# Performance work log

Hardware: AMD Instinct MI355X
Metric: run time of the kernel (lower is better)

## Reference

```python
import jax, jax.numpy as jnp
import numpy as np

ANCHOR = 32
STRIDE = 1
K_INIT = 16           # self.k  -> kernel = sqrt(k) = 4
KSEL = 1              # topk selects 1 region


def unfold(x, ksize, stride):
    # x: (N, C, H, W) -> (N, C*ksize*ksize, oh*ow), torch.F.unfold layout (C outermost)
    N, C, H, W = x.shape
    oh = (H - ksize) // stride + 1
    ow = (W - ksize) // stride + 1
    ih = stride * jnp.arange(oh)[:, None] + jnp.arange(ksize)[None, :]   # (oh, k)
    iw = stride * jnp.arange(ow)[:, None] + jnp.arange(ksize)[None, :]   # (ow, k)
    p = x[:, :, ih[:, None, :, None], iw[None, :, None, :]]             # (N,C,oh,ow,k,k)
    p = p.transpose(0, 1, 4, 5, 2, 3).reshape(N, C * ksize * ksize, oh * ow)
    return p


def min_max_norm(x):
    lo = x.min(axis=-1, keepdims=True)
    hi = x.max(axis=-1, keepdims=True)
    return (x - lo) / (hi - lo + 1e-5)


def perturbed_topk(scores, noise, sigma):
    # scores: (B, d); noise: (B, ns, d)  ->  indicators (B, KSEL, d)
    d = scores.shape[-1]
    pert = scores[:, None, :] + noise * sigma                # (B, ns, d)
    _, idx = jax.lax.top_k(pert, KSEL)                       # (B, ns, K)
    idx = jnp.sort(idx, axis=-1)
    oh = jax.nn.one_hot(idx, d, dtype=scores.dtype)          # (B, ns, K, d)
    return oh.mean(axis=1)                                   # (B, K, d)


def setup_inputs() -> dict:
    key = jax.random.key(0)
    k1, k2, k3, k4 = jax.random.split(key, 4)
    b, c, t, h, w = 2, 3, 8, 448, 448
    n_key, L = 4, 196
    num_region = 121            # ((14-4)//1 + 1)**2
    num_samples = 500
    x = jax.random.normal(k1, (b, c, t, h, w), dtype=jnp.float32)
    score = jax.random.uniform(k2, (b, n_key, L), dtype=jnp.float32)
    noise = jax.random.normal(k3, (b * n_key, num_samples, num_region), dtype=jnp.float32)
    sigma = jnp.float32(0.05)
    group_id = jax.random.randint(k4, (b, t), 0, n_key)
    return {"x": x, "score": score, "noise": noise, "sigma": sigma, "group_id": group_id}


def reference(x, score, noise, sigma, group_id):
    b, c, t, h, w = x.shape
    _, n_key, L = score.shape
    A = ANCHOR
    gh, gw = h // A, w // A                         # 14, 14 == sqrt(L): no interpolate
    s = int(np.sqrt(K_INIT))                        # 4

    score2 = score.reshape(b * n_key, 1, gh, gw)

    # rearrange 'b c t h w -> (b t) c h w', then space-to-depth by anchor
    xb = x.transpose(0, 2, 1, 3, 4).reshape(b * t, c, h, w)
    xb = xb.reshape(b * t, c, gh, A, gw, A).transpose(0, 1, 3, 5, 2, 4)
    xb = xb.reshape(b * t, c * A * A, gh, gw)

    xp = unfold(xb, s, STRIDE).transpose(0, 2, 1)   # (b*t, R, c*A*A*s*s)
    sc = unfold(score2, s, STRIDE).mean(axis=1)     # (b*n_key, R)
    sc = min_max_norm(sc)
    R = sc.shape[1]

    ind = perturbed_topk(sc, noise, sigma)          # (b*n_key, 1, R)
    ind = ind.transpose(0, 2, 1).reshape(b, n_key, R, 1)

    # extend indicator to every frame via its keyframe group id
    full = ind[jnp.arange(b)[:, None], group_id]    # (b, t, R, 1)
    full = full.reshape(b * t, R)

    # bmm(indicator^T, x): weighted (soft-selected) patch per frame
    patches = jnp.einsum('br,brc->bc', full, xp)    # (b*t, c*A*A*s*s)

    p = patches.reshape(b, t, c, A, A, s, s)
    p = p.transpose(0, 2, 1, 5, 3, 6, 4).reshape(b, c, t, s * A, s * A)
    return p
```

## Files before the change

### kernel.cpp

```cpp
#include <hip/hip_runtime.h>

#define BB 2
#define CC 3
#define TT 8
#define HW 448
#define AA 32
#define GG 14
#define RR 11
#define NR 121
#define NKEY 4
#define NS 500
#define NCH 25
#define SPC 20

typedef unsigned short u16;
typedef unsigned int u32;

__device__ __forceinline__ float bf2f(u16 u) {
  union { u32 i; float f; } v; v.i = ((u32)u) << 16; return v.f;
}
__device__ __forceinline__ u16 f2bf(float f) {
  union { float f; u32 i; } v; v.f = f;
  u32 u = v.i;
  return (u16)((u + 0x7fffu + ((u >> 16) & 1u)) >> 16);
}

__device__ __forceinline__ bool sniff_is_f32(const void* scorev) {
  const u16* sh16 = (const u16*)scorev;
  bool bf_ok = true;
#pragma unroll
  for (int i = 0; i < 16; i++) {
    const u16 v = sh16[i];
    if (!(v == 0 || (v >= 0x2000 && v <= 0x3F80))) bf_ok = false;
  }
  return !bf_ok;
}

__device__ __forceinline__ float read_sigma(const void* sigmav, bool is_f32) {
  const u32 w0 = *(const u32*)sigmav;
  if (is_f32) { union { u32 i; float f; } v; v.i = w0; return v.f; }
  float sg = bf2f((u16)(w0 & 0xffffu));
  union { u32 i; float f; } v; v.i = w0;
  if (!(sg > -100.f && sg < 100.f) && (v.f > -100.f && v.f < 100.f)) sg = v.f;
  return sg;
}

__global__ __launch_bounds__(128) void hist_part(
    const void* __restrict__ scorev, const void* __restrict__ noisev,
    const void* __restrict__ sigmav, int* __restrict__ wsp) {
  const int bk = blockIdx.x / NCH;
  const int ch = blockIdx.x % NCH;
  const int tid = threadIdx.x;

  __shared__ float nl[SPC * NR];
  __shared__ float scn[NR];
  __shared__ int hist[NR];
  __shared__ float lohi[2];

  const bool is_f32 = sniff_is_f32(scorev);
  const float sg = read_sigma(sigmav, is_f32);

  const size_t chunk_elem = (size_t)(bk * NS + ch * SPC) * NR;

  if (is_f32) {
    const float* nb = (const float*)noisev + chunk_elem;
    for (int i = tid; i < SPC * NR; i += 128) nl[i] = nb[i];
  } else {
    const u16* nb = (const u16*)noisev + chunk_elem;
    for (int i = tid; i < SPC * NR; i += 128) nl[i] = bf2f(nb[i]);
  }

  if (tid < NR) {
    hist[tid] = 0;
    const int oi = tid / RR, oj = tid - oi * RR;
    float ssum = 0.f;
    if (is_f32) {
      const float* sp = (const float*)scorev + bk * (GG * GG);
#pragma unroll
      for (int ki = 0; ki < 4; ki++)
#pragma unroll
        for (int kj = 0; kj < 4; kj++) ssum += sp[(oi + ki) * GG + (oj + kj)];
    } else {
      const u16* sp = (const u16*)scorev + bk * (GG * GG);
#pragma unroll
      for (int ki = 0; ki < 4; ki++)
#pragma unroll
        for (int kj = 0; kj < 4; kj++) ssum += bf2f(sp[(oi + ki) * GG + (oj + kj)]);
    }
    scn[tid] = ssum * 0.0625f;
  }
  __syncthreads();
  if (tid < 64) {
    float v1 = scn[tid];
    float v2 = (tid + 64 < NR) ? scn[tid + 64] : v1;
    float mn = fminf(v1, v2), mx = fmaxf(v1, v2);
#pragma unroll
    for (int off = 32; off > 0; off >>= 1) {
      mn = fminf(mn, __shfl_xor(mn, off, 64));
      mx = fmaxf(mx, __shfl_xor(mx, off, 64));
    }
    if (tid == 0) { lohi[0] = mn; lohi[1] = mx; }
  }
  __syncthreads();
  {
    const float lo = lohi[0];
    const float denom = lohi[1] - lo + 1e-5f;
    if (tid < NR) scn[tid] = (scn[tid] - lo) / denom;
  }
  __syncthreads();

  if (tid < SPC) {
    const float* npr = &nl[tid * NR];
    float bv = scn[0] + sg * npr[0];
    int bi = 0;
    for (int r = 1; r < NR; r++) {
      const float v = scn[r] + sg * npr[r];
      if (v > bv) { bv = v; bi = r; }
    }
    atomicAdd(&hist[bi], 1);
  }
  __syncthreads();

  if (tid < NR) {
    wsp[(bk * NCH + ch) * NR + tid] = hist[tid];
  }
}

__global__ __launch_bounds__(128) void gather_kernel(
    const void* __restrict__ xv, const void* __restrict__ scorev,
    const int* __restrict__ wsp, const int* __restrict__ group_id,
    void* __restrict__ outv) {
  int blk = blockIdx.x;
  const int a1 = blk & (AA - 1); blk >>= 5;
  const int t = blk % TT; blk /= TT;
  const int c = blk % CC; const int b = blk / CC;
  const int tid = threadIdx.x;

  __shared__ __align__(16) float xs[GG][HW];
  __shared__ float scn[NR];

  const bool is_f32 = sniff_is_f32(scorev);

  if (is_f32) {
    const float* xb = (const float*)xv + ((size_t)((b * CC + c) * TT + t)) * (HW * HW);
    for (int i = tid; i < GG * (HW / 4); i += 128) {
      const int g = i / (HW / 4);
      const int c4 = i - g * (HW / 4);
      *(float4*)(&xs[g][c4 * 4]) =
          *(const float4*)(xb + (size_t)(a1 + AA * g) * HW + c4 * 4);
    }
  } else {
    const u16* xb = (const u16*)xv + ((size_t)((b * CC + c) * TT + t)) * (HW * HW);
    for (int i = tid; i < GG * (HW / 8); i += 128) {
      const int g = i / (HW / 8);
      const int c8 = i - g * (HW / 8);
      const uint4 v = *(const uint4*)(xb + (size_t)(a1 + AA * g) * HW + c8 * 8);
      float* d = &xs[g][c8 * 8];
      d[0] = bf2f((u16)(v.x & 0xffffu)); d[1] = bf2f((u16)(v.x >> 16));
      d[2] = bf2f((u16)(v.y & 0xffffu)); d[3] = bf2f((u16)(v.y >> 16));
      d[4] = bf2f((u16)(v.z & 0xffffu)); d[5] = bf2f((u16)(v.z >> 16));
      d[6] = bf2f((u16)(v.w & 0xffffu)); d[7] = bf2f((u16)(v.w >> 16));
    }
  }

  if (tid < NR) {
    const int mybk = b * NKEY + group_id[b * TT + t];
    int acc = 0;
#pragma unroll
    for (int ch = 0; ch < NCH; ch++) {
      acc += wsp[(mybk * NCH + ch) * NR + tid];
    }
    scn[tid] = (float)acc * (1.0f / NS);
  }
  __syncthreads();

  const int ki = tid >> 5;
  const int j = (tid & 31) * 4;
  float acc0 = 0.f, acc1 = 0.f, acc2 = 0.f, acc3 = 0.f;
  for (int oi = 0; oi < RR; oi++) {
    const float* xrow = &xs[ki + oi][j];
    const float* wrow = &scn[oi * RR];
#pragma unroll
    for (int oj = 0; oj < RR; oj++) {
      const float wv = wrow[oj];
      const float4 v = *(const float4*)(xrow + AA * oj);
      acc0 += wv * v.x;
      acc1 += wv * v.y;
      acc2 += wv * v.z;
      acc3 += wv * v.w;
    }
  }

  const size_t obase =
      ((size_t)((b * CC + c) * TT + t) * 128 + (ki * AA + a1)) * 128 + j;
  if (is_f32) {
    float4 st; st.x = acc0; st.y = acc1; st.z = acc2; st.w = acc3;
    *(float4*)((float*)outv + obase) = st;
  } else {
    uint2 ov;
    ov.x = (u32)f2bf(acc0) | ((u32)f2bf(acc1) << 16);
    ov.y = (u32)f2bf(acc2) | ((u32)f2bf(acc3) << 16);
    *(uint2*)((u16*)outv + obase) = ov;
  }
}

extern "C" void kernel_launch(void* const* d_in, const int* in_sizes, int n_in,
                              void* d_out, int out_size, void* d_ws, size_t ws_size,
                              hipStream_t stream) {
  const void* x = d_in[0];
  const void* score = d_in[1];
  const void* noise = d_in[2];
  const void* sigma = d_in[3];
  const int* group_id = (const int*)d_in[4];
  (void)in_sizes; (void)n_in; (void)out_size; (void)ws_size;

  int* wsp = (int*)d_ws;

  hist_part<<<dim3(BB * NKEY * NCH), 128, 0, stream>>>(score, noise, sigma, wsp);
  gather_kernel<<<dim3(BB * CC * TT * AA), 128, 0, stream>>>(x, score, wsp,
                                                             group_id, d_out);
}
```

Before: 97.24 us.

## Restructure gather kernel to reuse each loaded x row across four output rows

Each block now handles two anchor rows with a single 64-thread wave, and each thread computes all four ki output rows at once. Every shared-memory x vector it reads feeds up to four accumulators instead of one, and the 121 weights are held in registers. This cuts redundant LDS reads and per-block overhead. In exchange it halves the block count, doubles the shared memory per block to about 50KB, and raises register pressure (31 float4 weights plus accumulators), which may lower occupancy and latency hiding during the global loads.

```diff
diff --git a/kernel.cpp b/kernel.cpp
--- a/kernel.cpp
+++ b/kernel.cpp
@@ -12,9 +12,11 @@
 #define NS 500
 #define NCH 25
 #define SPC 20
+#define XSH (GG * HW)
 
 typedef unsigned short u16;
 typedef unsigned int u32;
+typedef float f32x4 __attribute__((ext_vector_type(4)));
 
 __device__ __forceinline__ float bf2f(u16 u) {
   union { u32 i; float f; } v; v.i = ((u32)u) << 16; return v.f;
@@ -126,81 +128,110 @@
   }
 }
 
-__global__ __launch_bounds__(128) void gather_kernel(
+__global__ __launch_bounds__(64, 1) void gather_kernel(
     const void* __restrict__ xv, const void* __restrict__ scorev,
     const int* __restrict__ wsp, const int* __restrict__ group_id,
     void* __restrict__ outv) {
   int blk = blockIdx.x;
-  const int a1 = blk & (AA - 1); blk >>= 5;
+  const int p = blk & 15; blk >>= 4;
   const int t = blk % TT; blk /= TT;
   const int c = blk % CC; const int b = blk / CC;
   const int tid = threadIdx.x;
 
-  __shared__ __align__(16) float xs[GG][HW];
-  __shared__ float scn[NR];
+  __shared__ __align__(16) float xs[2 * XSH];
+  __shared__ __align__(16) float scn[124];
 
   const bool is_f32 = sniff_is_f32(scorev);
+  const int a1base = p * 2;
 
   if (is_f32) {
     const float* xb = (const float*)xv + ((size_t)((b * CC + c) * TT + t)) * (HW * HW);
-    for (int i = tid; i < GG * (HW / 4); i += 128) {
-      const int g = i / (HW / 4);
-      const int c4 = i - g * (HW / 4);
-      *(float4*)(&xs[g][c4 * 4]) =
-          *(const float4*)(xb + (size_t)(a1 + AA * g) * HW + c4 * 4);
+    for (int i = tid; i < 2 * GG * (HW / 4); i += 64) {
+      const int hh = i / (GG * (HW / 4));
+      const int rem = i - hh * (GG * (HW / 4));
+      const int g = rem / (HW / 4);
+      const int c4 = rem - g * (HW / 4);
+      *(f32x4*)&xs[hh * XSH + g * HW + c4 * 4] =
+          *(const f32x4*)((const float*)xb + (size_t)(a1base + hh + AA * g) * HW + c4 * 4);
     }
   } else {
     const u16* xb = (const u16*)xv + ((size_t)((b * CC + c) * TT + t)) * (HW * HW);
-    for (int i = tid; i < GG * (HW / 8); i += 128) {
-      const int g = i / (HW / 8);
-      const int c8 = i - g * (HW / 8);
-      const uint4 v = *(const uint4*)(xb + (size_t)(a1 + AA * g) * HW + c8 * 8);
-      float* d = &xs[g][c8 * 8];
-      d[0] = bf2f((u16)(v.x & 0xffffu)); d[1] = bf2f((u16)(v.x >> 16));
-      d[2] = bf2f((u16)(v.y & 0xffffu)); d[3] = bf2f((u16)(v.y >> 16));
-      d[4] = bf2f((u16)(v.z & 0xffffu)); d[5] = bf2f((u16)(v.z >> 16));
-      d[6] = bf2f((u16)(v.w & 0xffffu)); d[7] = bf2f((u16)(v.w >> 16));
-    }
-  }
-
-  if (tid < NR) {
+    for (int i = tid; i < 2 * GG * (HW / 8); i += 64) {
+      const int hh = i / (GG * (HW / 8));
+      const int rem = i - hh * (GG * (HW / 8));
+      const int g = rem / (HW / 8);
+      const int c8 = rem - g * (HW / 8);
+      const uint4 v = *(const uint4*)(xb + (size_t)(a1base + hh + AA * g) * HW + c8 * 8);
+      float* d = &xs[hh * XSH + g * HW + c8 * 8];
+      f32x4 lo, hi;
+      lo[0] = bf2f((u16)(v.x & 0xffffu)); lo[1] = bf2f((u16)(v.x >> 16));
+      lo[2] = bf2f((u16)(v.y & 0xffffu)); lo[3] = bf2f((u16)(v.y >> 16));
+      hi[0] = bf2f((u16)(v.z & 0xffffu)); hi[1] = bf2f((u16)(v.z >> 16));
+      hi[2] = bf2f((u16)(v.w & 0xffffu)); hi[3] = bf2f((u16)(v.w >> 16));
+      *(f32x4*)d = lo;
+      *(f32x4*)(d + 4) = hi;
+    }
+  }
+
+  {
     const int mybk = b * NKEY + group_id[b * TT + t];
-    int acc = 0;
-#pragma unroll
-    for (int ch = 0; ch < NCH; ch++) {
-      acc += wsp[(mybk * NCH + ch) * NR + tid];
-    }
-    scn[tid] = (float)acc * (1.0f / NS);
-  }
-  __syncthreads();
-
-  const int ki = tid >> 5;
+    for (int r = tid; r < NR; r += 64) {
+      int acc = 0;
+#pragma unroll
+      for (int ch = 0; ch < NCH; ch++) acc += wsp[(mybk * NCH + ch) * NR + r];
+      scn[r] = (float)acc * (1.0f / NS);
+    }
+    if (tid < 3) scn[NR + tid] = 0.f;
+  }
+  __syncthreads();
+
+  f32x4 w4[31];
+#pragma unroll
+  for (int q = 0; q < 31; q++) w4[q] = *(const f32x4*)&scn[4 * q];
+
+  const int h = tid >> 5;
   const int j = (tid & 31) * 4;
-  float acc0 = 0.f, acc1 = 0.f, acc2 = 0.f, acc3 = 0.f;
-  for (int oi = 0; oi < RR; oi++) {
-    const float* xrow = &xs[ki + oi][j];
-    const float* wrow = &scn[oi * RR];
+  const float* xh = &xs[h * XSH];
+
+  f32x4 q0 = 0.f, q1 = 0.f, q2 = 0.f, q3 = 0.f;
+
+#define WV(oi, oj) (w4[((oi) * RR + (oj)) >> 2][((oi) * RR + (oj)) & 3])
+#pragma unroll
+  for (int g = 0; g < GG; g++) {
 #pragma unroll
     for (int oj = 0; oj < RR; oj++) {
-      const float wv = wrow[oj];
-      const float4 v = *(const float4*)(xrow + AA * oj);
-      acc0 += wv * v.x;
-      acc1 += wv * v.y;
-      acc2 += wv * v.z;
-      acc3 += wv * v.w;
-    }
-  }
-
-  const size_t obase =
-      ((size_t)((b * CC + c) * TT + t) * 128 + (ki * AA + a1)) * 128 + j;
+      const f32x4 v = *(const f32x4*)(xh + g * HW + j + AA * oj);
+      if (g - 0 >= 0 && g - 0 < RR) q0 += WV(g - 0, oj) * v;
+      if (g - 1 >= 0 && g - 1 < RR) q1 += WV(g - 1, oj) * v;
+      if (g - 2 >= 0 && g - 2 < RR) q2 += WV(g - 2, oj) * v;
+      if (g - 3 >= 0 && g - 3 < RR) q3 += WV(g - 3, oj) * v;
+    }
+  }
+#undef WV
+
+  const int a1 = a1base + h;
+  const size_t rowbase = (size_t)((b * CC + c) * TT + t) * 128;
   if (is_f32) {
-    float4 st; st.x = acc0; st.y = acc1; st.z = acc2; st.w = acc3;
-    *(float4*)((float*)outv + obase) = st;
+    float* ob = (float*)outv;
+    *(f32x4*)&ob[(rowbase + (0 * AA + a1)) * 128 + j] = q0;
+    *(f32x4*)&ob[(rowbase + (1 * AA + a1)) * 128 + j] = q1;
+    *(f32x4*)&ob[(rowbase + (2 * AA + a1)) * 128 + j] = q2;
+    *(f32x4*)&ob[(rowbase + (3 * AA + a1)) * 128 + j] = q3;
   } else {
+    u16* ob = (u16*)outv;
     uint2 ov;
-    ov.x = (u32)f2bf(acc0) | ((u32)f2bf(acc1) << 16);
-    ov.y = (u32)f2bf(acc2) | ((u32)f2bf(acc3) << 16);
-    *(uint2*)((u16*)outv + obase) = ov;
+    ov.x = (u32)f2bf(q0[0]) | ((u32)f2bf(q0[1]) << 16);
+    ov.y = (u32)f2bf(q0[2]) | ((u32)f2bf(q0[3]) << 16);
+    *(uint2*)&ob[(rowbase + (0 * AA + a1)) * 128 + j] = ov;
+    ov.x = (u32)f2bf(q1[0]) | ((u32)f2bf(q1[1]) << 16);
+    ov.y = (u32)f2bf(q1[2]) | ((u32)f2bf(q1[3]) << 16);
+    *(uint2*)&ob[(rowbase + (1 * AA + a1)) * 128 + j] = ov;
+    ov.x = (u32)f2bf(q2[0]) | ((u32)f2bf(q2[1]) << 16);
+    ov.y = (u32)f2bf(q2[2]) | ((u32)f2bf(q2[3]) << 16);
+    *(uint2*)&ob[(rowbase + (2 * AA + a1)) * 128 + j] = ov;
+    ov.x = (u32)f2bf(q3[0]) | ((u32)f2bf(q3[1]) << 16);
+    ov.y = (u32)f2bf(q3[2]) | ((u32)f2bf(q3[3]) << 16);
+    *(uint2*)&ob[(rowbase + (3 * AA + a1)) * 128 + j] = ov;
   }
 }
 
@@ -217,6 +248,6 @@
   int* wsp = (int*)d_ws;
 
   hist_part<<<dim3(BB * NKEY * NCH), 128, 0, stream>>>(score, noise, sigma, wsp);
-  gather_kernel<<<dim3(BB * CC * TT * AA), 128, 0, stream>>>(x, score, wsp,
-                                                             group_id, d_out);
-}
+  gather_kernel<<<dim3(BB * CC * TT * (AA / 2)), 64, 0, stream>>>(x, score, wsp,
+                                                                  group_id, d_out);
+}
```

Measured after the change: 105.2 us. 8.2% more time.
